# Kernel optimization log

Hardware: AMD Instinct MI355X
Metric: run time of the kernel (lower is better)

The kernel has to match this reference:

```python
import jax, jax.numpy as jnp
import numpy as np

CHANNELS = 8
RADIUS = 2


def setup_inputs() -> dict:
    key = jax.random.key(0)
    k1, k2, k3 = jax.random.split(key, 3)
    x = jax.random.normal(k1, (4, CHANNELS + 1, 1024, 1024), dtype=jnp.float32)
    rand = jax.random.uniform(k2, (4, CHANNELS, 1024, 1024), dtype=jnp.float32)
    dropout_rand = jax.random.uniform(k3, (1024, 1024), dtype=jnp.float32)
    return {"x": x, "rand": rand, "dropout_rand": dropout_rand}


def reference(x, rand, dropout_rand):
    # x: [B, C+1, H, W]; spins in first C channels, inverse-temperature b in last.
    s = x[:, :CHANNELS]          # [B, C, H, W]
    b = x[:, -1:]                # [B, 1, H, W]

    # Cross-shaped stencil conv with all-ones weights shared across channels
    # (weight shape [1, C, Rk, Rk]): equivalent to summing over channels, then
    # summing circular rolls along the row and column of the cross. The circular
    # pad + valid conv is exactly a circular roll, so no padding is materialized.
    sc = s.sum(axis=1)           # [B, H, W]
    Js = sc  # center tap (weight 1, counted once)
    for d in range(1, RADIUS + 1):
        Js = Js + jnp.roll(sc, d, axis=-2) + jnp.roll(sc, -d, axis=-2)
        Js = Js + jnp.roll(sc, d, axis=-1) + jnp.roll(sc, -d, axis=-1)
    Js = Js[:, None]             # [B, 1, H, W], broadcasts over channels

    delta_e = 2.0 * s * Js       # [B, C, H, W]
    p = jnp.where(delta_e <= 0, jnp.ones_like(s), jnp.exp(-delta_e * b))
    dropout_mask = (dropout_rand > 0.5)[None, None]   # [1, 1, H, W]
    flip = 1.0 - 2.0 * ((rand < p) & dropout_mask).astype(s.dtype)
    return jnp.concatenate([s * flip, b], axis=1)
```

## Files before the change

kernel.cpp:

```cpp
#include <hip/hip_runtime.h>
#include <math.h>


#define NB 4
#define NC 8
#define HH 1024
#define WW 1024
#define PIX (HH * WW)

__device__ __forceinline__ float g4(const float4& v, int i) {
    return i == 0 ? v.x : i == 1 ? v.y : i == 2 ? v.z : v.w;
}
__device__ __forceinline__ void s4(float4& v, int i, float f) {
    if (i == 0) v.x = f; else if (i == 1) v.y = f; else if (i == 2) v.z = f; else v.w = f;
}

__global__ __launch_bounds__(256) void sc_kernel(const float* __restrict__ x,
                                                 float* __restrict__ sc) {
    int tid = blockIdx.x * 256 + threadIdx.x;
    int n   = tid >> 18;
    int g   = tid & ((PIX / 4) - 1);
    const float* base = x + (size_t)n * 9 * PIX + (size_t)g * 4;
    float4 s = *reinterpret_cast<const float4*>(base);
#pragma unroll
    for (int c = 1; c < NC; ++c) {
        float4 t = *reinterpret_cast<const float4*>(base + (size_t)c * PIX);
        s.x += t.x; s.y += t.y; s.z += t.z; s.w += t.w;
    }
    *reinterpret_cast<float4*>(sc + (size_t)n * PIX + (size_t)g * 4) = s;
}

__global__ __launch_bounds__(256) void ising_kernel(const float* __restrict__ x,
                                                    const float* __restrict__ rnd,
                                                    const float* __restrict__ dr,
                                                    const float* __restrict__ sc,
                                                    float* __restrict__ out) {
    int tid  = blockIdx.x * 256 + threadIdx.x;
    int n    = tid >> 18;
    int g    = tid & ((PIX / 4) - 1);
    int pix0 = g << 2;
    int y    = pix0 >> 10;
    int xc   = pix0 & (WW - 1);

    const float* scn = sc + (size_t)n * PIX;
    int ym1 = (y - 1) & (HH - 1), yp1 = (y + 1) & (HH - 1);
    int ym2 = (y - 2) & (HH - 1), yp2 = (y + 2) & (HH - 1);
    int xA  = (xc - 4) & (WW - 1);
    int xCq = (xc + 4) & (WW - 1);

    const float* xs = x   + (size_t)n * 9  * PIX + pix0;
    const float* rs = rnd + (size_t)n * NC * PIX + pix0;

    float4 sv[NC], rv[NC];
#pragma unroll
    for (int c = 0; c < NC; ++c)
        sv[c] = *reinterpret_cast<const float4*>(xs + (size_t)c * PIX);
#pragma unroll
    for (int c = 0; c < NC; ++c)
        rv[c] = *reinterpret_cast<const float4*>(rs + (size_t)c * PIX);
    float4 bv = *reinterpret_cast<const float4*>(xs + (size_t)NC * PIX);
    float4 dv = *reinterpret_cast<const float4*>(dr + pix0);

    float4 rB  = *reinterpret_cast<const float4*>(scn + (y   << 10) + xc);
    float4 rA  = *reinterpret_cast<const float4*>(scn + (y   << 10) + xA);
    float4 rC  = *reinterpret_cast<const float4*>(scn + (y   << 10) + xCq);
    float4 rM1 = *reinterpret_cast<const float4*>(scn + (ym1 << 10) + xc);
    float4 rP1 = *reinterpret_cast<const float4*>(scn + (yp1 << 10) + xc);
    float4 rM2 = *reinterpret_cast<const float4*>(scn + (ym2 << 10) + xc);
    float4 rP2 = *reinterpret_cast<const float4*>(scn + (yp2 << 10) + xc);

    float Js[4];
#pragma unroll
    for (int i = 0; i < 4; ++i) {
        float cen = g4(rB, i);
        float vy1m = g4(rM1, i), vy1p = g4(rP1, i);
        float vy2m = g4(rM2, i), vy2p = g4(rP2, i);
        float vx1m = (i == 0) ? g4(rA, 3) : g4(rB, i - 1);
        float vx1p = (i == 3) ? g4(rC, 0) : g4(rB, i + 1);
        float vx2m = (i < 2) ? g4(rA, 2 + i) : g4(rB, i - 2);
        float vx2p = (i < 2) ? g4(rB, i + 2) : g4(rC, i - 2);
        float j = cen;
        j = j + vy1m; j = j + vy1p;
        j = j + vx1m; j = j + vx1p;
        j = j + vy2m; j = j + vy2p;
        j = j + vx2m; j = j + vx2p;
        Js[i] = j;
    }

    bool dm[4];
#pragma unroll
    for (int i = 0; i < 4; ++i) dm[i] = g4(dv, i) > 0.5f;

    float* os = out + (size_t)n * 9 * PIX + pix0;
#pragma unroll
    for (int c = 0; c < NC; ++c) {
        float4 o;
#pragma unroll
        for (int i = 0; i < 4; ++i) {
            float s = g4(sv[c], i);
            float r = g4(rv[c], i);
            float de = (2.0f * s) * Js[i];
            float p = 1.0f;
            if (de > 0.0f) {
                float arg = (-de) * g4(bv, i);
                p = (float)exp((double)arg);
            }
            bool cond = (r < p) && dm[i];
            s4(o, i, cond ? -s : s);
        }
        *reinterpret_cast<float4*>(os + (size_t)c * PIX) = o;
    }
    *reinterpret_cast<float4*>(os + (size_t)NC * PIX) = bv;
}

extern "C" void kernel_launch(void* const* d_in, const int* in_sizes, int n_in,
                              void* d_out, int out_size, void* d_ws, size_t ws_size,
                              hipStream_t stream) {
    const float* x   = (const float*)d_in[0];
    const float* rnd = (const float*)d_in[1];
    const float* dr  = (const float*)d_in[2];
    float* out = (float*)d_out;
    float* sc  = (float*)d_ws;

    const int blocks = NB * PIX / 4 / 256;
    sc_kernel<<<blocks, 256, 0, stream>>>(x, sc);
    ising_kernel<<<blocks, 256, 0, stream>>>(x, rnd, dr, sc, out);
}
```

Measured before the change: 120.2 us.

## Use fast expf with guard band and double-precision fallback; nontemporal rand/out accesses

Replaces the unconditional double-precision exp with a fast __expf estimate plus a relative guard band. The exact double exp is computed only when some lane in the wavefront has rand inside the uncertain band. The change also streams the rand loads and output stores with nontemporal hints, and loads channels one per iteration instead of all up front to reduce register pressure. The aim is to cut the cost of fp64 transcendentals on a memory-bound kernel, at the price of wave-level divergence handling.

```diff
diff --git a/kernel.cpp b/kernel.cpp
--- a/kernel.cpp
+++ b/kernel.cpp
@@ -8,12 +8,7 @@
 #define WW 1024
 #define PIX (HH * WW)
 
-__device__ __forceinline__ float g4(const float4& v, int i) {
-    return i == 0 ? v.x : i == 1 ? v.y : i == 2 ? v.z : v.w;
-}
-__device__ __forceinline__ void s4(float4& v, int i, float f) {
-    if (i == 0) v.x = f; else if (i == 1) v.y = f; else if (i == 2) v.z = f; else v.w = f;
-}
+typedef float f32x4 __attribute__((ext_vector_type(4)));
 
 __global__ __launch_bounds__(256) void sc_kernel(const float* __restrict__ x,
                                                  float* __restrict__ sc) {
@@ -21,13 +16,13 @@
     int n   = tid >> 18;
     int g   = tid & ((PIX / 4) - 1);
     const float* base = x + (size_t)n * 9 * PIX + (size_t)g * 4;
-    float4 s = *reinterpret_cast<const float4*>(base);
+    f32x4 s = *reinterpret_cast<const f32x4*>(base);
 #pragma unroll
     for (int c = 1; c < NC; ++c) {
-        float4 t = *reinterpret_cast<const float4*>(base + (size_t)c * PIX);
-        s.x += t.x; s.y += t.y; s.z += t.z; s.w += t.w;
+        f32x4 t = *reinterpret_cast<const f32x4*>(base + (size_t)c * PIX);
+        s = s + t;
     }
-    *reinterpret_cast<float4*>(sc + (size_t)n * PIX + (size_t)g * 4) = s;
+    *reinterpret_cast<f32x4*>(sc + (size_t)n * PIX + (size_t)g * 4) = s;
 }
 
 __global__ __launch_bounds__(256) void ising_kernel(const float* __restrict__ x,
@@ -48,37 +43,24 @@
     int xA  = (xc - 4) & (WW - 1);
     int xCq = (xc + 4) & (WW - 1);
 
-    const float* xs = x   + (size_t)n * 9  * PIX + pix0;
-    const float* rs = rnd + (size_t)n * NC * PIX + pix0;
-
-    float4 sv[NC], rv[NC];
-#pragma unroll
-    for (int c = 0; c < NC; ++c)
-        sv[c] = *reinterpret_cast<const float4*>(xs + (size_t)c * PIX);
-#pragma unroll
-    for (int c = 0; c < NC; ++c)
-        rv[c] = *reinterpret_cast<const float4*>(rs + (size_t)c * PIX);
-    float4 bv = *reinterpret_cast<const float4*>(xs + (size_t)NC * PIX);
-    float4 dv = *reinterpret_cast<const float4*>(dr + pix0);
-
-    float4 rB  = *reinterpret_cast<const float4*>(scn + (y   << 10) + xc);
-    float4 rA  = *reinterpret_cast<const float4*>(scn + (y   << 10) + xA);
-    float4 rC  = *reinterpret_cast<const float4*>(scn + (y   << 10) + xCq);
-    float4 rM1 = *reinterpret_cast<const float4*>(scn + (ym1 << 10) + xc);
-    float4 rP1 = *reinterpret_cast<const float4*>(scn + (yp1 << 10) + xc);
-    float4 rM2 = *reinterpret_cast<const float4*>(scn + (ym2 << 10) + xc);
-    float4 rP2 = *reinterpret_cast<const float4*>(scn + (yp2 << 10) + xc);
+    f32x4 rB  = *reinterpret_cast<const f32x4*>(scn + (y   << 10) + xc);
+    f32x4 rA  = *reinterpret_cast<const f32x4*>(scn + (y   << 10) + xA);
+    f32x4 rC  = *reinterpret_cast<const f32x4*>(scn + (y   << 10) + xCq);
+    f32x4 rM1 = *reinterpret_cast<const f32x4*>(scn + (ym1 << 10) + xc);
+    f32x4 rP1 = *reinterpret_cast<const f32x4*>(scn + (yp1 << 10) + xc);
+    f32x4 rM2 = *reinterpret_cast<const f32x4*>(scn + (ym2 << 10) + xc);
+    f32x4 rP2 = *reinterpret_cast<const f32x4*>(scn + (yp2 << 10) + xc);
 
     float Js[4];
 #pragma unroll
     for (int i = 0; i < 4; ++i) {
-        float cen = g4(rB, i);
-        float vy1m = g4(rM1, i), vy1p = g4(rP1, i);
-        float vy2m = g4(rM2, i), vy2p = g4(rP2, i);
-        float vx1m = (i == 0) ? g4(rA, 3) : g4(rB, i - 1);
-        float vx1p = (i == 3) ? g4(rC, 0) : g4(rB, i + 1);
-        float vx2m = (i < 2) ? g4(rA, 2 + i) : g4(rB, i - 2);
-        float vx2p = (i < 2) ? g4(rB, i + 2) : g4(rC, i - 2);
+        float cen  = rB[i];
+        float vy1m = rM1[i], vy1p = rP1[i];
+        float vy2m = rM2[i], vy2p = rP2[i];
+        float vx1m = (i == 0) ? rA[3] : rB[i - 1];
+        float vx1p = (i == 3) ? rC[0] : rB[i + 1];
+        float vx2m = (i < 2) ? rA[2 + i] : rB[i - 2];
+        float vx2p = (i < 2) ? rB[i + 2] : rC[i - 2];
         float j = cen;
         j = j + vy1m; j = j + vy1p;
         j = j + vx1m; j = j + vx1p;
@@ -87,30 +69,61 @@
         Js[i] = j;
     }
 
+    const float* xs = x   + (size_t)n * 9  * PIX + pix0;
+    const float* rs = rnd + (size_t)n * NC * PIX + pix0;
+    float*       os = out + (size_t)n * 9  * PIX + pix0;
+
+    f32x4 bv = *reinterpret_cast<const f32x4*>(xs + (size_t)NC * PIX);
+    f32x4 dv = *reinterpret_cast<const f32x4*>(dr + pix0);
     bool dm[4];
 #pragma unroll
-    for (int i = 0; i < 4; ++i) dm[i] = g4(dv, i) > 0.5f;
+    for (int i = 0; i < 4; ++i) dm[i] = dv[i] > 0.5f;
 
-    float* os = out + (size_t)n * 9 * PIX + pix0;
 #pragma unroll
     for (int c = 0; c < NC; ++c) {
-        float4 o;
+        f32x4 sv = *reinterpret_cast<const f32x4*>(xs + (size_t)c * PIX);
+        f32x4 rv = __builtin_nontemporal_load(
+                        reinterpret_cast<const f32x4*>(rs + (size_t)c * PIX));
+        float de[4], arg[4];
+        bool fastlow[4], und[4];
+        bool anyund = false;
 #pragma unroll
         for (int i = 0; i < 4; ++i) {
-            float s = g4(sv[c], i);
-            float r = g4(rv[c], i);
-            float de = (2.0f * s) * Js[i];
-            float p = 1.0f;
-            if (de > 0.0f) {
-                float arg = (-de) * g4(bv, i);
-                p = (float)exp((double)arg);
+            float s = sv[i], r = rv[i];
+            de[i]  = (2.0f * s) * Js[i];
+            arg[i] = (-de[i]) * bv[i];
+            float pa   = __expf(arg[i]);
+            float band = pa * 4.0e-5f;
+            float lo   = pa - band;
+            float hi   = pa + band;
+            bool  fl = r < lo;
+            bool  fh = r > hi;
+            fastlow[i] = fl;
+            und[i] = (de[i] > 0.0f) && !fl && !fh;
+            anyund = anyund || und[i];
+        }
+        f32x4 o;
+        if (__any(anyund)) {
+#pragma unroll
+            for (int i = 0; i < 4; ++i) {
+                float s = sv[i], r = rv[i];
+                bool take;
+                if (de[i] <= 0.0f)  take = true;
+                else if (und[i])    take = r < (float)exp((double)arg[i]);
+                else                take = fastlow[i];
+                o[i] = (take && dm[i]) ? -s : s;
             }
-            bool cond = (r < p) && dm[i];
-            s4(o, i, cond ? -s : s);
+        } else {
+#pragma unroll
+            for (int i = 0; i < 4; ++i) {
+                float s = sv[i];
+                bool take = (de[i] <= 0.0f) || fastlow[i];
+                o[i] = (take && dm[i]) ? -s : s;
+            }
         }
-        *reinterpret_cast<float4*>(os + (size_t)c * PIX) = o;
+        __builtin_nontemporal_store(o, reinterpret_cast<f32x4*>(os + (size_t)c * PIX));
     }
-    *reinterpret_cast<float4*>(os + (size_t)NC * PIX) = bv;
+    __builtin_nontemporal_store(bv, reinterpret_cast<f32x4*>(os + (size_t)NC * PIX));
 }
 
 extern "C" void kernel_launch(void* const* d_in, const int* in_sizes, int n_in,
```

New measurement: 108.6 us. -9.7%, faster.
